# Kernel tuning notes

Measured on AMD Instinct MI355X. Metric: run time of the kernel, lower is better.

## Reference

```python
import jax, jax.numpy as jnp
import numpy as np

# Complete binary tree: node 0 is the root, node i's parent is (i-1)//2.
# adjacency[i, j] = 1 iff j is the parent of i (matches _parent_indices/_child_indices).
N_LEVELS = 11
N_LABELS = 2 ** N_LEVELS - 1  # 2047
N_CLASSES = 2
BATCH = 2048


def _tree_structure():
    # levels[t]: node ids at tree level t (root level 0)
    levels = [np.arange(2 ** t - 1, 2 ** (t + 1) - 1) for t in range(N_LEVELS)]
    parent = np.zeros(N_LABELS, dtype=np.int64)
    parent[1:] = (np.arange(1, N_LABELS) - 1) // 2
    return levels, parent


def _propagate(emissions, transitions, edge_layers):
    """Belief-propagation sweep. edge_layers is a list (per depth, in order)
    of (src, dst) numpy index arrays: each src node sends a message to dst.
    Message: m[b, c_dst, dst] += logsumexp_{c_src}(emissions[b,c_src,src]
              + messages[b,c_src,src] + transitions[dst, src, c_dst, c_src]).
    Identical math to (Batched)MessagePassing.forward, expressed per edge.
    """
    messages = jnp.zeros_like(emissions)
    for src, dst in edge_layers:
        e = emissions[:, :, src] + messages[:, :, src]           # [B, Cs, E]
        t = transitions[dst, src]                                 # [E, Cd, Cs]
        # elem[b, cd, e, cs] = e[b, cs, e] + t[e, cd, cs]
        elem = e.transpose(0, 2, 1)[:, None, :, :] + t.transpose(1, 0, 2)[None]
        contrib = jax.nn.logsumexp(elem, axis=-1)                 # [B, Cd, E]
        messages = messages.at[:, :, dst].add(contrib)
    return messages


def setup_inputs() -> dict:
    key = jax.random.key(0)
    k1, k2 = jax.random.split(key)
    emissions = jax.random.normal(k1, (BATCH, N_CLASSES, N_LABELS), dtype=jnp.float32)
    transitions = jax.random.normal(k2, (N_LABELS, N_LABELS, N_CLASSES, N_CLASSES), dtype=jnp.float32)
    return {"emissions": emissions, "transitions": transitions}


def reference(emissions, transitions):
    levels, parent = _tree_structure()
    # upward (alphas): leaves -> root, successor = parent
    up_edges = [(levels[t], parent[levels[t]]) for t in range(N_LEVELS - 1, 0, -1)]
    # downward (betas): root -> leaves, successor = child
    down_edges = [(parent[levels[t]], levels[t]) for t in range(1, N_LEVELS)]
    alphas = _propagate(emissions, transitions, up_edges)
    betas = _propagate(emissions, transitions, down_edges)
    scores = emissions + alphas + betas                           # [B, C, L]
    # normalize over classes per label -> marginal log-probabilities
    return scores - jax.nn.logsumexp(scores, axis=1, keepdims=True)
```

## Files before the change

kernel.cpp:

```cpp
#include <hip/hip_runtime.h>


#define N_LEVELS 11
#define N_LABELS 2047
#define BATCH    2048
#define NTHREADS 256

__device__ __forceinline__ float lse2(float x, float y) {
    float m = fmaxf(x, y);
    float d = fminf(x, y) - m;
    return m + __logf(1.0f + __expf(d));
}

__global__ __launch_bounds__(NTHREADS) void treecrf_kernel(
    const float* __restrict__ emissions,
    const float* __restrict__ transitions,
    float* __restrict__ out)
{
    __shared__ float em[2 * N_LABELS];
    __shared__ float alphas[2 * N_LABELS];
    __shared__ float betas[2 * N_LABELS];

    const int b = blockIdx.x;
    const int tid = threadIdx.x;
    const float* emg = emissions + (size_t)b * (2 * N_LABELS);
    float* outg = out + (size_t)b * (2 * N_LABELS);
    const float4* tr4 = (const float4*)transitions;

    {
        const float2* src = (const float2*)emg;
        float2* dst = (float2*)em;
        for (int i = tid; i < N_LABELS; i += NTHREADS) dst[i] = src[i];
    }
    for (int i = tid; i < 1024; i += NTHREADS) {
        alphas[1023 + i] = 0.f;
        alphas[N_LABELS + 1023 + i] = 0.f;
    }
    __syncthreads();

    for (int lvl = N_LEVELS - 2; lvl >= 0; --lvl) {
        const int base = (1 << lvl) - 1;
        const int n = 1 << lvl;
        for (int off = tid; off < n; off += NTHREADS) {
            const int p = base + off;
            const int c0 = 2 * p + 1, c1 = c0 + 1;
            const float a00 = em[c0] + alphas[c0];
            const float a01 = em[N_LABELS + c0] + alphas[N_LABELS + c0];
            const float a10 = em[c1] + alphas[c1];
            const float a11 = em[N_LABELS + c1] + alphas[N_LABELS + c1];
            const float4 t0 = tr4[p * N_LABELS + c0];
            const float4 t1 = tr4[p * N_LABELS + c1];
            alphas[p]            = lse2(a00 + t0.x, a01 + t0.y)
                                 + lse2(a10 + t1.x, a11 + t1.y);
            alphas[N_LABELS + p] = lse2(a00 + t0.z, a01 + t0.w)
                                 + lse2(a10 + t1.z, a11 + t1.w);
        }
        __syncthreads();
    }

    if (tid == 0) {
        betas[0] = 0.f; betas[N_LABELS] = 0.f;
        const float s0 = em[0] + alphas[0];
        const float s1 = em[N_LABELS] + alphas[N_LABELS];
        const float l = lse2(s0, s1);
        outg[0] = s0 - l;
        outg[N_LABELS] = s1 - l;
    }
    __syncthreads();

    for (int lvl = 1; lvl < N_LEVELS; ++lvl) {
        const int base = (1 << lvl) - 1;
        const int n = 1 << lvl;
        for (int off = tid; off < n; off += NTHREADS) {
            const int i = base + off;
            const int p = (i - 1) >> 1;
            const float b0 = em[p] + betas[p];
            const float b1 = em[N_LABELS + p] + betas[N_LABELS + p];
            const float4 t = tr4[i * N_LABELS + p];
            const float v0 = lse2(b0 + t.x, b1 + t.y);
            const float v1 = lse2(b0 + t.z, b1 + t.w);
            betas[i] = v0;
            betas[N_LABELS + i] = v1;
            const float s0 = em[i] + alphas[i] + v0;
            const float s1 = em[N_LABELS + i] + alphas[N_LABELS + i] + v1;
            const float l = lse2(s0, s1);
            outg[i] = s0 - l;
            outg[N_LABELS + i] = s1 - l;
        }
        __syncthreads();
    }
}

extern "C" void kernel_launch(void* const* d_in, const int* in_sizes, int n_in,
                              void* d_out, int out_size, void* d_ws, size_t ws_size,
                              hipStream_t stream) {
    const float* emissions   = (const float*)d_in[0];
    const float* transitions = (const float*)d_in[1];
    float* out = (float*)d_out;
    treecrf_kernel<<<BATCH, NTHREADS, 0, stream>>>(emissions, transitions, out);
}
```

Measured before the change: 161.8 us.

## Rewrite tree CRF as one wavefront per batch with register-resident subtrees and packed transitions

Replaces the 256-thread block with shared-memory level sweeps by a 64-lane kernel where each lane owns a 16-leaf subtree in registers. The top six levels are combined with cross-lane shuffles, so no shared memory or block barriers are needed. A small pre-kernel gathers the needed transition entries into a coalesced slot-major table in the workspace. Emission loads and output stores are vectorised. This is meant to remove the barrier and scattered-load costs, in exchange for high register pressure and an extra kernel launch.

```diff
diff --git a/kernel.cpp b/kernel.cpp
--- a/kernel.cpp
+++ b/kernel.cpp
@@ -1,101 +1,252 @@
 #include <hip/hip_runtime.h>
 
 
-#define N_LEVELS 11
-#define N_LABELS 2047
-#define BATCH    2048
-#define NTHREADS 256
+#define L 2047
+#define NSLOTS 78
+
+typedef float __attribute__((ext_vector_type(4), aligned(4))) uf4;
+typedef float __attribute__((ext_vector_type(2), aligned(4))) uf2;
 
 __device__ __forceinline__ float lse2(float x, float y) {
     float m = fmaxf(x, y);
-    float d = fminf(x, y) - m;
-    return m + __logf(1.0f + __expf(d));
-}
-
-__global__ __launch_bounds__(NTHREADS) void treecrf_kernel(
+    return m + __logf(1.0f + __expf(fminf(x, y) - m));
+}
+
+__device__ __forceinline__ void up_pair(float c00, float c01, float c10, float c11,
+                                        float4 tA, float4 tB, float em0, float em1,
+                                        float& o0, float& o1) {
+    o0 = em0 + lse2(c00 + tA.x, c01 + tA.y) + lse2(c10 + tB.x, c11 + tB.y);
+    o1 = em1 + lse2(c00 + tA.z, c01 + tA.w) + lse2(c10 + tB.z, c11 + tB.w);
+}
+
+__device__ __forceinline__ void slot_decode(int s, int l, int& node, int& src) {
+    if (s < 16)      { int p = 511 + 8*l + (s >> 1); node = p; src = 2*p + 1 + (s & 1); }
+    else if (s < 24) { int j = s - 16; int p = 255 + 4*l + (j >> 1); node = p; src = 2*p + 1 + (j & 1); }
+    else if (s < 28) { int j = s - 24; int p = 127 + 2*l + (j >> 1); node = p; src = 2*p + 1 + (j & 1); }
+    else if (s < 30) { int j = s - 28; int p = 63 + l; node = p; src = 2*p + 1 + j; }
+    else if (s < 42) { int d = (s - 30) >> 1; int r = (s - 30) & 1;
+                       int P = (1 << (5 - d)) - 1 + (l >> (d + 1)); node = P; src = 2*P + 1 + r; }
+    else if (s < 47) { int t = s - 41; int n = (1 << t) - 1 + (l >> (6 - t)); node = n; src = (n - 1) >> 1; }
+    else if (s < 48) { int n = 63 + l; node = n; src = (n - 1) >> 1; }
+    else if (s < 50) { int j = s - 48; int n = 127 + 2*l + j; node = n; src = (n - 1) >> 1; }
+    else if (s < 54) { int j = s - 50; int n = 255 + 4*l + j; node = n; src = (n - 1) >> 1; }
+    else if (s < 62) { int j = s - 54; int n = 511 + 8*l + j; node = n; src = (n - 1) >> 1; }
+    else             { int j = s - 62; int n = 1023 + 16*l + j; node = n; src = (n - 1) >> 1; }
+}
+
+__device__ __forceinline__ float4 ldT(const float4* __restrict__ pk,
+                                      const float4* __restrict__ tr4, int s, int l) {
+    if (pk) return pk[(s << 6) + l];
+    int n, c; slot_decode(s, l, n, c);
+    return tr4[n * L + c];
+}
+
+__global__ void pack_kernel(const float4* __restrict__ tr4, float4* __restrict__ packed) {
+    int idx = blockIdx.x * 256 + threadIdx.x;
+    if (idx >= NSLOTS * 64) return;
+    int s = idx >> 6, l = idx & 63;
+    int n, c; slot_decode(s, l, n, c);
+    packed[idx] = tr4[n * L + c];
+}
+
+__global__ __launch_bounds__(64) void treecrf_main(
     const float* __restrict__ emissions,
-    const float* __restrict__ transitions,
+    const float4* __restrict__ pk,
+    const float4* __restrict__ tr4,
     float* __restrict__ out)
 {
-    __shared__ float em[2 * N_LABELS];
-    __shared__ float alphas[2 * N_LABELS];
-    __shared__ float betas[2 * N_LABELS];
-
+    const int l = threadIdx.x;
     const int b = blockIdx.x;
-    const int tid = threadIdx.x;
-    const float* emg = emissions + (size_t)b * (2 * N_LABELS);
-    float* outg = out + (size_t)b * (2 * N_LABELS);
-    const float4* tr4 = (const float4*)transitions;
-
-    {
-        const float2* src = (const float2*)emg;
-        float2* dst = (float2*)em;
-        for (int i = tid; i < N_LABELS; i += NTHREADS) dst[i] = src[i];
-    }
-    for (int i = tid; i < 1024; i += NTHREADS) {
-        alphas[1023 + i] = 0.f;
-        alphas[N_LABELS + 1023 + i] = 0.f;
-    }
-    __syncthreads();
-
-    for (int lvl = N_LEVELS - 2; lvl >= 0; --lvl) {
-        const int base = (1 << lvl) - 1;
-        const int n = 1 << lvl;
-        for (int off = tid; off < n; off += NTHREADS) {
-            const int p = base + off;
-            const int c0 = 2 * p + 1, c1 = c0 + 1;
-            const float a00 = em[c0] + alphas[c0];
-            const float a01 = em[N_LABELS + c0] + alphas[N_LABELS + c0];
-            const float a10 = em[c1] + alphas[c1];
-            const float a11 = em[N_LABELS + c1] + alphas[N_LABELS + c1];
-            const float4 t0 = tr4[p * N_LABELS + c0];
-            const float4 t1 = tr4[p * N_LABELS + c1];
-            alphas[p]            = lse2(a00 + t0.x, a01 + t0.y)
-                                 + lse2(a10 + t1.x, a11 + t1.y);
-            alphas[N_LABELS + p] = lse2(a00 + t0.z, a01 + t0.w)
-                                 + lse2(a10 + t1.z, a11 + t1.w);
-        }
-        __syncthreads();
-    }
-
-    if (tid == 0) {
-        betas[0] = 0.f; betas[N_LABELS] = 0.f;
-        const float s0 = em[0] + alphas[0];
-        const float s1 = em[N_LABELS] + alphas[N_LABELS];
-        const float l = lse2(s0, s1);
-        outg[0] = s0 - l;
-        outg[N_LABELS] = s1 - l;
-    }
-    __syncthreads();
-
-    for (int lvl = 1; lvl < N_LEVELS; ++lvl) {
-        const int base = (1 << lvl) - 1;
-        const int n = 1 << lvl;
-        for (int off = tid; off < n; off += NTHREADS) {
-            const int i = base + off;
-            const int p = (i - 1) >> 1;
-            const float b0 = em[p] + betas[p];
-            const float b1 = em[N_LABELS + p] + betas[N_LABELS + p];
-            const float4 t = tr4[i * N_LABELS + p];
-            const float v0 = lse2(b0 + t.x, b1 + t.y);
-            const float v1 = lse2(b0 + t.z, b1 + t.w);
-            betas[i] = v0;
-            betas[N_LABELS + i] = v1;
-            const float s0 = em[i] + alphas[i] + v0;
-            const float s1 = em[N_LABELS + i] + alphas[N_LABELS + i] + v1;
-            const float l = lse2(s0, s1);
-            outg[i] = s0 - l;
-            outg[N_LABELS + i] = s1 - l;
-        }
-        __syncthreads();
+    const float* __restrict__ e0 = emissions + (size_t)b * (2 * L);
+    const float* __restrict__ e1 = e0 + L;
+    float* __restrict__ o0 = out + (size_t)b * (2 * L);
+    float* __restrict__ o1 = o0 + L;
+
+    float el0[16], el1[16];
+    {
+        const uf4* p0 = (const uf4*)(e0 + 1023 + 16 * l);
+        const uf4* p1 = (const uf4*)(e1 + 1023 + 16 * l);
+        #pragma unroll
+        for (int k = 0; k < 4; ++k) {
+            uf4 a = p0[k], c = p1[k];
+            el0[4*k] = a.x; el0[4*k+1] = a.y; el0[4*k+2] = a.z; el0[4*k+3] = a.w;
+            el1[4*k] = c.x; el1[4*k+1] = c.y; el1[4*k+2] = c.z; el1[4*k+3] = c.w;
+        }
+    }
+    float em9_0[8], em9_1[8], em8_0[4], em8_1[4], em7_0[2], em7_1[2], em6_0, em6_1;
+    {
+        const uf4* p0 = (const uf4*)(e0 + 511 + 8 * l);
+        const uf4* p1 = (const uf4*)(e1 + 511 + 8 * l);
+        uf4 a = p0[0], bq = p0[1], c = p1[0], d = p1[1];
+        em9_0[0]=a.x; em9_0[1]=a.y; em9_0[2]=a.z; em9_0[3]=a.w;
+        em9_0[4]=bq.x; em9_0[5]=bq.y; em9_0[6]=bq.z; em9_0[7]=bq.w;
+        em9_1[0]=c.x; em9_1[1]=c.y; em9_1[2]=c.z; em9_1[3]=c.w;
+        em9_1[4]=d.x; em9_1[5]=d.y; em9_1[6]=d.z; em9_1[7]=d.w;
+        uf4 e = *(const uf4*)(e0 + 255 + 4 * l);
+        uf4 f = *(const uf4*)(e1 + 255 + 4 * l);
+        em8_0[0]=e.x; em8_0[1]=e.y; em8_0[2]=e.z; em8_0[3]=e.w;
+        em8_1[0]=f.x; em8_1[1]=f.y; em8_1[2]=f.z; em8_1[3]=f.w;
+        uf2 g = *(const uf2*)(e0 + 127 + 2 * l);
+        uf2 h = *(const uf2*)(e1 + 127 + 2 * l);
+        em7_0[0]=g.x; em7_0[1]=g.y; em7_1[0]=h.x; em7_1[1]=h.y;
+        em6_0 = e0[63 + l]; em6_1 = e1[63 + l];
+    }
+
+    float A9_0[8], A9_1[8];
+    #pragma unroll
+    for (int j = 0; j < 8; ++j) {
+        float4 tA = ldT(pk, tr4, 2*j, l), tB = ldT(pk, tr4, 2*j + 1, l);
+        up_pair(el0[2*j], el1[2*j], el0[2*j+1], el1[2*j+1], tA, tB,
+                em9_0[j], em9_1[j], A9_0[j], A9_1[j]);
+    }
+    float A8_0[4], A8_1[4];
+    #pragma unroll
+    for (int j = 0; j < 4; ++j) {
+        float4 tA = ldT(pk, tr4, 16 + 2*j, l), tB = ldT(pk, tr4, 17 + 2*j, l);
+        up_pair(A9_0[2*j], A9_1[2*j], A9_0[2*j+1], A9_1[2*j+1], tA, tB,
+                em8_0[j], em8_1[j], A8_0[j], A8_1[j]);
+    }
+    float A7_0[2], A7_1[2];
+    #pragma unroll
+    for (int j = 0; j < 2; ++j) {
+        float4 tA = ldT(pk, tr4, 24 + 2*j, l), tB = ldT(pk, tr4, 25 + 2*j, l);
+        up_pair(A8_0[2*j], A8_1[2*j], A8_0[2*j+1], A8_1[2*j+1], tA, tB,
+                em7_0[j], em7_1[j], A7_0[j], A7_1[j]);
+    }
+    float A6_0, A6_1;
+    {
+        float4 tA = ldT(pk, tr4, 28, l), tB = ldT(pk, tr4, 29, l);
+        up_pair(A7_0[0], A7_1[0], A7_0[1], A7_1[1], tA, tB, em6_0, em6_1, A6_0, A6_1);
+    }
+
+    float cur0 = A6_0, cur1 = A6_1;
+    float Aa0[6], Aa1[6], Ea0[6], Ea1[6];
+    #pragma unroll
+    for (int d = 0; d < 6; ++d) {
+        const int t = 5 - d;
+        const int P = (1 << t) - 1 + (l >> (d + 1));
+        float p0v = __shfl_xor(cur0, 1 << d);
+        float p1v = __shfl_xor(cur1, 1 << d);
+        bool isL = ((l >> d) & 1) == 0;
+        float L0 = isL ? cur0 : p0v, L1 = isL ? cur1 : p1v;
+        float R0 = isL ? p0v : cur0, R1 = isL ? p1v : cur1;
+        float4 tL = ldT(pk, tr4, 30 + 2*d, l), tR = ldT(pk, tr4, 31 + 2*d, l);
+        float eP0 = e0[P], eP1 = e1[P];
+        up_pair(L0, L1, R0, R1, tL, tR, eP0, eP1, cur0, cur1);
+        Aa0[t] = cur0; Aa1[t] = cur1; Ea0[t] = eP0; Ea1[t] = eP1;
+    }
+
+    if (l == 0) {
+        float m = lse2(cur0, cur1);
+        o0[0] = cur0 - m; o1[0] = cur1 - m;
+    }
+    float D0 = Ea0[0], D1 = Ea1[0];
+
+    #pragma unroll
+    for (int t = 1; t <= 5; ++t) {
+        const int n = (1 << t) - 1 + (l >> (6 - t));
+        float4 td = ldT(pk, tr4, 41 + t, l);
+        float b0 = lse2(D0 + td.x, D1 + td.y);
+        float b1 = lse2(D0 + td.z, D1 + td.w);
+        float s0 = Aa0[t] + b0, s1 = Aa1[t] + b1;
+        float m = lse2(s0, s1);
+        if ((l & ((1 << (6 - t)) - 1)) == 0) { o0[n] = s0 - m; o1[n] = s1 - m; }
+        D0 = Ea0[t] + b0; D1 = Ea1[t] + b1;
+    }
+
+    {
+        float4 td = ldT(pk, tr4, 47, l);
+        float b0 = lse2(D0 + td.x, D1 + td.y);
+        float b1 = lse2(D0 + td.z, D1 + td.w);
+        float s0 = A6_0 + b0, s1 = A6_1 + b1, m = lse2(s0, s1);
+        o0[63 + l] = s0 - m; o1[63 + l] = s1 - m;
+        D0 = em6_0 + b0; D1 = em6_1 + b1;
+    }
+
+    float D7_0[2], D7_1[2];
+    {
+        float w0[2], w1[2];
+        #pragma unroll
+        for (int j = 0; j < 2; ++j) {
+            float4 td = ldT(pk, tr4, 48 + j, l);
+            float b0 = lse2(D0 + td.x, D1 + td.y);
+            float b1 = lse2(D0 + td.z, D1 + td.w);
+            float s0 = A7_0[j] + b0, s1 = A7_1[j] + b1, m = lse2(s0, s1);
+            w0[j] = s0 - m; w1[j] = s1 - m;
+            D7_0[j] = em7_0[j] + b0; D7_1[j] = em7_1[j] + b1;
+        }
+        *(uf2*)(o0 + 127 + 2*l) = uf2{w0[0], w0[1]};
+        *(uf2*)(o1 + 127 + 2*l) = uf2{w1[0], w1[1]};
+    }
+
+    float D8_0[4], D8_1[4];
+    {
+        float w0[4], w1[4];
+        #pragma unroll
+        for (int j = 0; j < 4; ++j) {
+            float4 td = ldT(pk, tr4, 50 + j, l);
+            float b0 = lse2(D7_0[j>>1] + td.x, D7_1[j>>1] + td.y);
+            float b1 = lse2(D7_0[j>>1] + td.z, D7_1[j>>1] + td.w);
+            float s0 = A8_0[j] + b0, s1 = A8_1[j] + b1, m = lse2(s0, s1);
+            w0[j] = s0 - m; w1[j] = s1 - m;
+            D8_0[j] = em8_0[j] + b0; D8_1[j] = em8_1[j] + b1;
+        }
+        *(uf4*)(o0 + 255 + 4*l) = uf4{w0[0], w0[1], w0[2], w0[3]};
+        *(uf4*)(o1 + 255 + 4*l) = uf4{w1[0], w1[1], w1[2], w1[3]};
+    }
+
+    float D9_0[8], D9_1[8];
+    {
+        float w0[8], w1[8];
+        #pragma unroll
+        for (int j = 0; j < 8; ++j) {
+            float4 td = ldT(pk, tr4, 54 + j, l);
+            float b0 = lse2(D8_0[j>>1] + td.x, D8_1[j>>1] + td.y);
+            float b1 = lse2(D8_0[j>>1] + td.z, D8_1[j>>1] + td.w);
+            float s0 = A9_0[j] + b0, s1 = A9_1[j] + b1, m = lse2(s0, s1);
+            w0[j] = s0 - m; w1[j] = s1 - m;
+            D9_0[j] = em9_0[j] + b0; D9_1[j] = em9_1[j] + b1;
+        }
+        uf4* q0 = (uf4*)(o0 + 511 + 8*l);
+        uf4* q1 = (uf4*)(o1 + 511 + 8*l);
+        q0[0] = uf4{w0[0], w0[1], w0[2], w0[3]}; q0[1] = uf4{w0[4], w0[5], w0[6], w0[7]};
+        q1[0] = uf4{w1[0], w1[1], w1[2], w1[3]}; q1[1] = uf4{w1[4], w1[5], w1[6], w1[7]};
+    }
+
+    {
+        float w0[16], w1[16];
+        #pragma unroll
+        for (int k = 0; k < 16; ++k) {
+            float4 td = ldT(pk, tr4, 62 + k, l);
+            float b0 = lse2(D9_0[k>>1] + td.x, D9_1[k>>1] + td.y);
+            float b1 = lse2(D9_0[k>>1] + td.z, D9_1[k>>1] + td.w);
+            float s0 = el0[k] + (A9_0[k>>1] - em9_0[k>>1], 0.f), s1;
+            s0 = el0[k] + b0; s1 = el1[k] + b1;
+            float m = lse2(s0, s1);
+            w0[k] = s0 - m; w1[k] = s1 - m;
+        }
+        uf4* q0 = (uf4*)(o0 + 1023 + 16*l);
+        uf4* q1 = (uf4*)(o1 + 1023 + 16*l);
+        #pragma unroll
+        for (int k = 0; k < 4; ++k) {
+            q0[k] = uf4{w0[4*k], w0[4*k+1], w0[4*k+2], w0[4*k+3]};
+            q1[k] = uf4{w1[4*k], w1[4*k+1], w1[4*k+2], w1[4*k+3]};
+        }
     }
 }
 
 extern "C" void kernel_launch(void* const* d_in, const int* in_sizes, int n_in,
                               void* d_out, int out_size, void* d_ws, size_t ws_size,
                               hipStream_t stream) {
-    const float* emissions   = (const float*)d_in[0];
-    const float* transitions = (const float*)d_in[1];
+    const float* emissions = (const float*)d_in[0];
+    const float4* tr4 = (const float4*)d_in[1];
     float* out = (float*)d_out;
-    treecrf_kernel<<<BATCH, NTHREADS, 0, stream>>>(emissions, transitions, out);
-}
+
+    const size_t packed_bytes = (size_t)NSLOTS * 64 * sizeof(float4);
+    const bool use_ws = (ws_size >= packed_bytes) && (d_ws != nullptr);
+    float4* pk = use_ws ? (float4*)d_ws : nullptr;
+    if (use_ws) {
+        pack_kernel<<<(NSLOTS * 64 + 255) / 256, 256, 0, stream>>>(tr4, pk);
+    }
+    treecrf_main<<<2048, 64, 0, stream>>>(emissions, pk, tr4, out);
+}
```

After: 138.5 us. -14.4%, faster.
